# Performance work log

Hardware: AMD Instinct MI355X
Metric: run time of the kernel (lower is better)

Reference implementation:

```python
import jax, jax.numpy as jnp
import numpy as np

FH = FW = 3

def _decomp_layer(x, f0, f1, f2, f3):
    # x: (B, C, H, W); f0: (F, r), f1: (FH, r), f2: (FW, r), f3: (C, r)
    B, C, H, W = x.shape
    Ho, Wo = H - FH + 1, W - FW + 1
    # unfold -> patches (B, C, Ho, Wo, FH, FW); fixed 3x3 loop, not a data-dim loop
    patches = jnp.stack(
        [jnp.stack([x[:, :, i:i + Ho, j:j + Wo] for j in range(FW)], axis=-1)
         for i in range(FH)], axis=-2)
    # permute to (B, Ho, Wo, FH, FW, C) as in torch's permute(0,2,3,4,5,1)
    patches = patches.transpose(0, 2, 3, 4, 5, 1)
    # CP contraction: collapse fh, fw, c against rank factors, then expand to filters
    t = jnp.einsum('bhwxyc,xr,yr,cr->bhwr', patches, f1, f2, f3)
    return jnp.einsum('bhwr,fr->bfhw', t, f0)  # (B, F, Ho, Wo)


def setup_inputs() -> dict:
    key = jax.random.key(0)
    ks = jax.random.split(key, 12)
    B, C, H, W = 512, 3, 32, 32
    F, R, NC = 32, 16, 10
    s = 0.1
    return {
        'x': jax.random.normal(ks[0], (B, C, H, W), jnp.float32),
        'l1_f0': jax.random.normal(ks[1], (F, R), jnp.float32) * s,
        'l1_f1': jax.random.normal(ks[2], (FH, R), jnp.float32) * s,
        'l1_f2': jax.random.normal(ks[3], (FW, R), jnp.float32) * s,
        'l1_f3': jax.random.normal(ks[4], (C, R), jnp.float32) * s,
        'l2_f0': jax.random.normal(ks[5], (F, R), jnp.float32) * s,
        'l2_f1': jax.random.normal(ks[6], (FH, R), jnp.float32) * s,
        'l2_f2': jax.random.normal(ks[7], (FW, R), jnp.float32) * s,
        'l2_f3': jax.random.normal(ks[8], (F, R), jnp.float32) * s,
        'W_cls': jax.random.normal(ks[9], (NC, 25088), jnp.float32) * 0.01,
        'b_cls': jnp.zeros((NC,), jnp.float32),
    }


def reference(x, l1_f0, l1_f1, l1_f2, l1_f3, l2_f0, l2_f1, l2_f2, l2_f3, W_cls, b_cls):
    h = _decomp_layer(x, l1_f0, l1_f1, l1_f2, l1_f3)        # (B, 32, 30, 30)
    h = _decomp_layer(h, l2_f0, l2_f1, l2_f2, l2_f3)        # (B, 32, 28, 28)
    h = h.reshape(h.shape[0], -1)                            # (B, 25088)
    logits = h @ W_cls.T + b_cls
    return jax.nn.log_softmax(logits, axis=1)
```

## Files before the change

kernel.cpp:

```cpp
#include <hip/hip_runtime.h>
#include <math.h>


#define NT 1024

__global__ void precomp_kernel(const float* __restrict__ l1_f0,
                               const float* __restrict__ l2_f0,
                               const float* __restrict__ l2_f3,
                               const float* __restrict__ Wcls,
                               float* __restrict__ Wc2,
                               float* __restrict__ Mm) {
    int id = blockIdx.x * blockDim.x + threadIdx.x;
    if (id < 10 * 16 * 784) {
        int n = id / (16 * 784);
        int rem = id - n * (16 * 784);
        int r2 = rem / 784;
        int pix = rem - r2 * 784;
        float acc = 0.f;
#pragma unroll
        for (int f = 0; f < 32; ++f)
            acc += l2_f0[f * 16 + r2] * Wcls[n * 25088 + f * 784 + pix];
        Wc2[id] = acc;
    }
    if (id < 256) {
        int r1 = id >> 4, r2 = id & 15;
        float acc = 0.f;
#pragma unroll
        for (int f = 0; f < 32; ++f)
            acc += l1_f0[f * 16 + r1] * l2_f3[f * 16 + r2];
        Mm[id] = acc;
    }
}

__global__ __launch_bounds__(NT) void fused_kernel(
    const float* __restrict__ x,
    const float* __restrict__ l1_f1, const float* __restrict__ l1_f2,
    const float* __restrict__ l1_f3,
    const float* __restrict__ l2_f1, const float* __restrict__ l2_f2,
    const float* __restrict__ Wc2, const float* __restrict__ Mm,
    const float* __restrict__ b_cls,
    float* __restrict__ out) {
    __shared__ float sA[16 * 1024];
    __shared__ float sB[16 * 900];
    __shared__ float sw1[144];
    __shared__ float sw2[144];
    __shared__ float sf3[48];
    __shared__ float sM[256];
    __shared__ float sred[16 * 10];
    __shared__ float slog[10];

    const int tid = threadIdx.x;
    const int b = blockIdx.x;

    if (tid < 48) sf3[tid] = l1_f3[tid];
    if (tid < 144) {
        int r = tid / 9, ij = tid - r * 9;
        int i = ij / 3, j = ij - i * 3;
        sw1[tid] = l1_f1[i * 16 + r] * l1_f2[j * 16 + r];
    }
    if (tid >= 144 && tid < 288) {
        int t = tid - 144;
        int r = t / 9, ij = t - r * 9;
        int i = ij / 3, j = ij - i * 3;
        sw2[t] = l2_f1[i * 16 + r] * l2_f2[j * 16 + r];
    }
    if (tid >= 288 && tid < 544) sM[tid - 288] = Mm[tid - 288];
    __syncthreads();

    {
        const int p = tid;
        float x0 = x[b * 3072 + p];
        float x1 = x[b * 3072 + 1024 + p];
        float x2 = x[b * 3072 + 2048 + p];
#pragma unroll
        for (int r = 0; r < 16; ++r)
            sA[r * 1024 + p] = x0 * sf3[r] + x1 * sf3[16 + r] + x2 * sf3[32 + r];
    }
    __syncthreads();

    {
        const int r = tid >> 6;
        const int s = tid & 63;
        const int col = s & 31;
        const int half = s >> 5;
        if (col < 30) {
            const float* wp = &sw1[r * 9];
            float w0 = wp[0], w1 = wp[1], w2 = wp[2];
            float w3 = wp[3], w4 = wp[4], w5 = wp[5];
            float w6 = wp[6], w7 = wp[7], w8 = wp[8];
            const int ho0 = half * 15;
            const float* base = &sA[r * 1024 + ho0 * 32 + col];
            float a0 = base[0],  a1 = base[1],  a2 = base[2];
            float b0 = base[32], b1 = base[33], b2 = base[34];
            float* op = &sB[r * 900 + ho0 * 30 + col];
#pragma unroll
            for (int step = 0; step < 15; ++step) {
                const float* rp = base + (step + 2) * 32;
                float c0 = rp[0], c1 = rp[1], c2 = rp[2];
                float acc = w0 * a0 + w1 * a1 + w2 * a2
                          + w3 * b0 + w4 * b1 + w5 * b2
                          + w6 * c0 + w7 * c1 + w8 * c2;
                op[step * 30] = acc;
                a0 = b0; a1 = b1; a2 = b2;
                b0 = c0; b1 = c1; b2 = c2;
            }
        }
    }
    __syncthreads();

    {
        if (tid < 900) {
            const int tile_r = tid & 3;
            const int tile_p = tid >> 2;
            const int r2b = tile_r * 4;
            const int p4 = tile_p * 4;
            float acc0x = 0.f, acc0y = 0.f, acc0z = 0.f, acc0w = 0.f;
            float acc1x = 0.f, acc1y = 0.f, acc1z = 0.f, acc1w = 0.f;
            float acc2x = 0.f, acc2y = 0.f, acc2z = 0.f, acc2w = 0.f;
            float acc3x = 0.f, acc3y = 0.f, acc3z = 0.f, acc3w = 0.f;
#pragma unroll
            for (int r1 = 0; r1 < 16; ++r1) {
                float4 tv = *(const float4*)&sB[r1 * 900 + p4];
                float4 mv = *(const float4*)&sM[r1 * 16 + r2b];
                acc0x += mv.x * tv.x; acc0y += mv.x * tv.y; acc0z += mv.x * tv.z; acc0w += mv.x * tv.w;
                acc1x += mv.y * tv.x; acc1y += mv.y * tv.y; acc1z += mv.y * tv.z; acc1w += mv.y * tv.w;
                acc2x += mv.z * tv.x; acc2y += mv.z * tv.y; acc2z += mv.z * tv.z; acc2w += mv.z * tv.w;
                acc3x += mv.w * tv.x; acc3y += mv.w * tv.y; acc3z += mv.w * tv.z; acc3w += mv.w * tv.w;
            }
            *(float4*)&sA[(r2b + 0) * 900 + p4] = make_float4(acc0x, acc0y, acc0z, acc0w);
            *(float4*)&sA[(r2b + 1) * 900 + p4] = make_float4(acc1x, acc1y, acc1z, acc1w);
            *(float4*)&sA[(r2b + 2) * 900 + p4] = make_float4(acc2x, acc2y, acc2z, acc2w);
            *(float4*)&sA[(r2b + 3) * 900 + p4] = make_float4(acc3x, acc3y, acc3z, acc3w);
        }
    }
    __syncthreads();

    {
        const int r2 = tid >> 6;
        const int s = tid & 63;
        const int col = s & 31;
        const int half = s >> 5;
        if (col < 28) {
            const float* wp = &sw2[r2 * 9];
            float w0 = wp[0], w1 = wp[1], w2 = wp[2];
            float w3 = wp[3], w4 = wp[4], w5 = wp[5];
            float w6 = wp[6], w7 = wp[7], w8 = wp[8];
            const int ho0 = half * 14;
            const float* base = &sA[r2 * 900 + ho0 * 30 + col];
            float a0 = base[0],  a1 = base[1],  a2 = base[2];
            float b0 = base[30], b1 = base[31], b2 = base[32];
            float* op = &sB[r2 * 784 + ho0 * 28 + col];
#pragma unroll
            for (int step = 0; step < 14; ++step) {
                const float* rp = base + (step + 2) * 30;
                float c0 = rp[0], c1 = rp[1], c2 = rp[2];
                float acc = w0 * a0 + w1 * a1 + w2 * a2
                          + w3 * b0 + w4 * b1 + w5 * b2
                          + w6 * c0 + w7 * c1 + w8 * c2;
                op[step * 28] = acc;
                a0 = b0; a1 = b1; a2 = b2;
                b0 = c0; b1 = c1; b2 = c2;
            }
        }
    }
    __syncthreads();

    float acc[10];
#pragma unroll
    for (int n = 0; n < 10; ++n) acc[n] = 0.f;
    for (int q = tid; q < 3136; q += NT) {
        float4 tv = *(const float4*)&sB[q * 4];
#pragma unroll
        for (int n = 0; n < 10; ++n) {
            float4 wv = *(const float4*)&Wc2[n * 12544 + q * 4];
            acc[n] += tv.x * wv.x + tv.y * wv.y + tv.z * wv.z + tv.w * wv.w;
        }
    }
#pragma unroll
    for (int n = 0; n < 10; ++n) {
        float v = acc[n];
        for (int off = 32; off > 0; off >>= 1)
            v += __shfl_down(v, off, 64);
        if ((tid & 63) == 0) sred[(tid >> 6) * 10 + n] = v;
    }
    __syncthreads();
    if (tid < 10) {
        float lg = b_cls[tid];
#pragma unroll
        for (int w = 0; w < 16; ++w) lg += sred[w * 10 + tid];
        slog[tid] = lg;
    }
    __syncthreads();
    if (tid < 10) {
        float m = -1e30f;
#pragma unroll
        for (int n = 0; n < 10; ++n) m = fmaxf(m, slog[n]);
        float s = 0.f;
#pragma unroll
        for (int n = 0; n < 10; ++n) s += expf(slog[n] - m);
        out[b * 10 + tid] = slog[tid] - m - logf(s);
    }
}

extern "C" void kernel_launch(void* const* d_in, const int* in_sizes, int n_in,
                              void* d_out, int out_size, void* d_ws, size_t ws_size,
                              hipStream_t stream) {
    const float* x     = (const float*)d_in[0];
    const float* l1_f0 = (const float*)d_in[1];
    const float* l1_f1 = (const float*)d_in[2];
    const float* l1_f2 = (const float*)d_in[3];
    const float* l1_f3 = (const float*)d_in[4];
    const float* l2_f0 = (const float*)d_in[5];
    const float* l2_f1 = (const float*)d_in[6];
    const float* l2_f2 = (const float*)d_in[7];
    const float* l2_f3 = (const float*)d_in[8];
    const float* Wcls  = (const float*)d_in[9];
    const float* bcls  = (const float*)d_in[10];
    float* out = (float*)d_out;

    float* Wc2 = (float*)d_ws;
    float* Mm  = Wc2 + 10 * 16 * 784;

    precomp_kernel<<<dim3((10 * 16 * 784 + 255) / 256), dim3(256), 0, stream>>>(
        l1_f0, l2_f0, l2_f3, Wcls, Wc2, Mm);
    fused_kernel<<<dim3(512), dim3(NT), 0, stream>>>(
        x, l1_f1, l1_f2, l1_f3, l2_f1, l2_f2, Wc2, Mm, bcls, out);
}
```

Measured before the change: 105.5 us.

## Fuse channel projection into conv1 and classifier dot into conv2, shrink LDS

Stores the raw input as float4 per pixel and applies the channel-rank projection on the fly inside the first 3x3 depthwise stage, which removes the 16x1024 intermediate buffer. The second depthwise stage now feeds its outputs straight into the classifier dot product with Wc2, dropping the separate shared-memory pass and one barrier. The rank-mixing matmul is retiled to 2 pixels by 16 ranks per thread and writes in place. LDS per block falls from about 124KB to about 75KB, and launch_bounds now asks for a minimum of 8 waves per EU. The costs are extra projection FMAs for the overlapping taps, unvectorized global reads of Wc2, and more register pressure.

New measurement: 226.6 us. 2.15x slower.

```diff
diff --git a/kernel.cpp b/kernel.cpp
--- a/kernel.cpp
+++ b/kernel.cpp
@@ -32,7 +32,7 @@
     }
 }
 
-__global__ __launch_bounds__(NT) void fused_kernel(
+__global__ __launch_bounds__(NT, 8) void fused_kernel(
     const float* __restrict__ x,
     const float* __restrict__ l1_f1, const float* __restrict__ l1_f2,
     const float* __restrict__ l1_f3,
@@ -40,8 +40,8 @@
     const float* __restrict__ Wc2, const float* __restrict__ Mm,
     const float* __restrict__ b_cls,
     float* __restrict__ out) {
-    __shared__ float sA[16 * 1024];
-    __shared__ float sB[16 * 900];
+    __shared__ float4 sx[1024];
+    __shared__ float st[16 * 900];
     __shared__ float sw1[144];
     __shared__ float sw2[144];
     __shared__ float sf3[48];
@@ -52,30 +52,27 @@
     const int tid = threadIdx.x;
     const int b = blockIdx.x;
 
+    {
+        const float* xb = x + b * 3072;
+        float x0 = xb[tid];
+        float x1 = xb[1024 + tid];
+        float x2 = xb[2048 + tid];
+        sx[tid] = make_float4(x0, x1, x2, 0.f);
+    }
     if (tid < 48) sf3[tid] = l1_f3[tid];
-    if (tid < 144) {
-        int r = tid / 9, ij = tid - r * 9;
+    if (tid >= 64 && tid < 208) {
+        int t = tid - 64;
+        int r = t / 9, ij = t - r * 9;
         int i = ij / 3, j = ij - i * 3;
-        sw1[tid] = l1_f1[i * 16 + r] * l1_f2[j * 16 + r];
-    }
-    if (tid >= 144 && tid < 288) {
-        int t = tid - 144;
+        sw1[t] = l1_f1[i * 16 + r] * l1_f2[j * 16 + r];
+    }
+    if (tid >= 256 && tid < 400) {
+        int t = tid - 256;
         int r = t / 9, ij = t - r * 9;
         int i = ij / 3, j = ij - i * 3;
         sw2[t] = l2_f1[i * 16 + r] * l2_f2[j * 16 + r];
     }
-    if (tid >= 288 && tid < 544) sM[tid - 288] = Mm[tid - 288];
-    __syncthreads();
-
-    {
-        const int p = tid;
-        float x0 = x[b * 3072 + p];
-        float x1 = x[b * 3072 + 1024 + p];
-        float x2 = x[b * 3072 + 2048 + p];
-#pragma unroll
-        for (int r = 0; r < 16; ++r)
-            sA[r * 1024 + p] = x0 * sf3[r] + x1 * sf3[16 + r] + x2 * sf3[32 + r];
-    }
+    if (tid >= 512 && tid < 768) sM[tid - 512] = Mm[tid - 512];
     __syncthreads();
 
     {
@@ -84,19 +81,21 @@
         const int col = s & 31;
         const int half = s >> 5;
         if (col < 30) {
+            const float f30 = sf3[r], f31 = sf3[16 + r], f32 = sf3[32 + r];
             const float* wp = &sw1[r * 9];
             float w0 = wp[0], w1 = wp[1], w2 = wp[2];
             float w3 = wp[3], w4 = wp[4], w5 = wp[5];
             float w6 = wp[6], w7 = wp[7], w8 = wp[8];
             const int ho0 = half * 15;
-            const float* base = &sA[r * 1024 + ho0 * 32 + col];
-            float a0 = base[0],  a1 = base[1],  a2 = base[2];
-            float b0 = base[32], b1 = base[33], b2 = base[34];
-            float* op = &sB[r * 900 + ho0 * 30 + col];
+            const float4* xb = &sx[ho0 * 32 + col];
+#define TAP(idx) ({ float4 _v = xb[(idx)]; _v.x * f30 + _v.y * f31 + _v.z * f32; })
+            float a0 = TAP(0),  a1 = TAP(1),  a2 = TAP(2);
+            float b0 = TAP(32), b1 = TAP(33), b2 = TAP(34);
+            float* op = &st[r * 900 + ho0 * 30 + col];
 #pragma unroll
             for (int step = 0; step < 15; ++step) {
-                const float* rp = base + (step + 2) * 32;
-                float c0 = rp[0], c1 = rp[1], c2 = rp[2];
+                const int nb = (step + 2) * 32;
+                float c0 = TAP(nb), c1 = TAP(nb + 1), c2 = TAP(nb + 2);
                 float acc = w0 * a0 + w1 * a1 + w2 * a2
                           + w3 * b0 + w4 * b1 + w5 * b2
                           + w6 * c0 + w7 * c1 + w8 * c2;
@@ -104,37 +103,37 @@
                 a0 = b0; a1 = b1; a2 = b2;
                 b0 = c0; b1 = c1; b2 = c2;
             }
+#undef TAP
         }
     }
     __syncthreads();
 
-    {
-        if (tid < 900) {
-            const int tile_r = tid & 3;
-            const int tile_p = tid >> 2;
-            const int r2b = tile_r * 4;
-            const int p4 = tile_p * 4;
-            float acc0x = 0.f, acc0y = 0.f, acc0z = 0.f, acc0w = 0.f;
-            float acc1x = 0.f, acc1y = 0.f, acc1z = 0.f, acc1w = 0.f;
-            float acc2x = 0.f, acc2y = 0.f, acc2z = 0.f, acc2w = 0.f;
-            float acc3x = 0.f, acc3y = 0.f, acc3z = 0.f, acc3w = 0.f;
-#pragma unroll
-            for (int r1 = 0; r1 < 16; ++r1) {
-                float4 tv = *(const float4*)&sB[r1 * 900 + p4];
-                float4 mv = *(const float4*)&sM[r1 * 16 + r2b];
-                acc0x += mv.x * tv.x; acc0y += mv.x * tv.y; acc0z += mv.x * tv.z; acc0w += mv.x * tv.w;
-                acc1x += mv.y * tv.x; acc1y += mv.y * tv.y; acc1z += mv.y * tv.z; acc1w += mv.y * tv.w;
-                acc2x += mv.z * tv.x; acc2y += mv.z * tv.y; acc2z += mv.z * tv.z; acc2w += mv.z * tv.w;
-                acc3x += mv.w * tv.x; acc3y += mv.w * tv.y; acc3z += mv.w * tv.z; acc3w += mv.w * tv.w;
+    if (tid < 450) {
+        const int p2 = tid * 2;
+        float acc0[16], acc1[16];
+#pragma unroll
+        for (int r2 = 0; r2 < 16; ++r2) { acc0[r2] = 0.f; acc1[r2] = 0.f; }
+#pragma unroll
+        for (int r1 = 0; r1 < 16; ++r1) {
+            float2 tv = *(const float2*)&st[r1 * 900 + p2];
+#pragma unroll
+            for (int q = 0; q < 4; ++q) {
+                float4 mv = *(const float4*)&sM[r1 * 16 + q * 4];
+                acc0[q * 4 + 0] += mv.x * tv.x;  acc1[q * 4 + 0] += mv.x * tv.y;
+                acc0[q * 4 + 1] += mv.y * tv.x;  acc1[q * 4 + 1] += mv.y * tv.y;
+                acc0[q * 4 + 2] += mv.z * tv.x;  acc1[q * 4 + 2] += mv.z * tv.y;
+                acc0[q * 4 + 3] += mv.w * tv.x;  acc1[q * 4 + 3] += mv.w * tv.y;
             }
-            *(float4*)&sA[(r2b + 0) * 900 + p4] = make_float4(acc0x, acc0y, acc0z, acc0w);
-            *(float4*)&sA[(r2b + 1) * 900 + p4] = make_float4(acc1x, acc1y, acc1z, acc1w);
-            *(float4*)&sA[(r2b + 2) * 900 + p4] = make_float4(acc2x, acc2y, acc2z, acc2w);
-            *(float4*)&sA[(r2b + 3) * 900 + p4] = make_float4(acc3x, acc3y, acc3z, acc3w);
         }
-    }
-    __syncthreads();
-
+#pragma unroll
+        for (int r2 = 0; r2 < 16; ++r2)
+            *(float2*)&st[r2 * 900 + p2] = make_float2(acc0[r2], acc1[r2]);
+    }
+    __syncthreads();
+
+    float acc[10];
+#pragma unroll
+    for (int n = 0; n < 10; ++n) acc[n] = 0.f;
     {
         const int r2 = tid >> 6;
         const int s = tid & 63;
@@ -146,36 +145,27 @@
             float w3 = wp[3], w4 = wp[4], w5 = wp[5];
             float w6 = wp[6], w7 = wp[7], w8 = wp[8];
             const int ho0 = half * 14;
-            const float* base = &sA[r2 * 900 + ho0 * 30 + col];
+            const float* base = &st[r2 * 900 + ho0 * 30 + col];
             float a0 = base[0],  a1 = base[1],  a2 = base[2];
             float b0 = base[30], b1 = base[31], b2 = base[32];
-            float* op = &sB[r2 * 784 + ho0 * 28 + col];
+            const float* wc = &Wc2[r2 * 784 + ho0 * 28 + col];
 #pragma unroll
             for (int step = 0; step < 14; ++step) {
                 const float* rp = base + (step + 2) * 30;
                 float c0 = rp[0], c1 = rp[1], c2 = rp[2];
-                float acc = w0 * a0 + w1 * a1 + w2 * a2
-                          + w3 * b0 + w4 * b1 + w5 * b2
-                          + w6 * c0 + w7 * c1 + w8 * c2;
-                op[step * 28] = acc;
+                float v = w0 * a0 + w1 * a1 + w2 * a2
+                        + w3 * b0 + w4 * b1 + w5 * b2
+                        + w6 * c0 + w7 * c1 + w8 * c2;
+                const float* wq = wc + step * 28;
+#pragma unroll
+                for (int n = 0; n < 10; ++n)
+                    acc[n] += v * wq[n * 12544];
                 a0 = b0; a1 = b1; a2 = b2;
                 b0 = c0; b1 = c1; b2 = c2;
             }
         }
     }
-    __syncthreads();
-
-    float acc[10];
-#pragma unroll
-    for (int n = 0; n < 10; ++n) acc[n] = 0.f;
-    for (int q = tid; q < 3136; q += NT) {
-        float4 tv = *(const float4*)&sB[q * 4];
-#pragma unroll
-        for (int n = 0; n < 10; ++n) {
-            float4 wv = *(const float4*)&Wc2[n * 12544 + q * 4];
-            acc[n] += tv.x * wv.x + tv.y * wv.y + tv.z * wv.z + tv.w * wv.w;
-        }
-    }
+
 #pragma unroll
     for (int n = 0; n < 10; ++n) {
         float v = acc[n];
@@ -195,10 +185,10 @@
         float m = -1e30f;
 #pragma unroll
         for (int n = 0; n < 10; ++n) m = fmaxf(m, slog[n]);
-        float s = 0.f;
-#pragma unroll
-        for (int n = 0; n < 10; ++n) s += expf(slog[n] - m);
-        out[b * 10 + tid] = slog[tid] - m - logf(s);
+        float ssum = 0.f;
+#pragma unroll
+        for (int n = 0; n < 10; ++n) ssum += expf(slog[n] - m);
+        out[b * 10 + tid] = slog[tid] - m - logf(ssum);
     }
 }
 
```
